# Performance work log

Hardware: AMD Instinct MI355X
Metric: run time of the kernel (lower is better)

The kernel has to match this reference:

```python
import jax, jax.numpy as jnp
import numpy as np

N, C_IN, C_OUT = 16384, 512, 1024

def setup_inputs() -> dict:
    key = jax.random.key(0)
    k1, k2 = jax.random.split(key)
    x = jax.random.normal(k1, (N, C_IN), dtype=jnp.float32)
    mean = jax.random.normal(k2, (C_OUT, C_IN), dtype=jnp.float32)
    return {"x": x, "mean": mean}

def reference(x, mean):
    # out[n, o] = 1 / sqrt(sum_c (x[n,c] - mean[o,c])^2)
    x_sq = jnp.sum(x * x, axis=-1, keepdims=True)            # [N, 1]
    m_sq = jnp.sum(mean * mean, axis=-1)                     # [O]
    cross = jnp.einsum('nc,oc->no', x, mean)                 # [N, O] GEMM
    d2 = x_sq - 2.0 * cross + m_sq[None, :]                  # [N, O]
    return jax.lax.rsqrt(d2)
```

## Files before the change

### kernel.cpp

```cpp
#include <hip/hip_runtime.h>
#include <hip/hip_bf16.h>
#include <stdint.h>

#define N_ROWS 16384
#define O_ROWS 1024
#define K_DIM  512

typedef __bf16 bf16x8 __attribute__((ext_vector_type(8)));
typedef float  f32x4  __attribute__((ext_vector_type(4)));

__device__ __forceinline__ ushort f2bfu(float f) {
    __bf16 h = (__bf16)f;
    return __builtin_bit_cast(ushort, h);
}

#define BAR_LGKM()  do {                                        \
    asm volatile("s_waitcnt lgkmcnt(0)" ::: "memory");          \
    __builtin_amdgcn_s_barrier();                               \
} while (0)

__global__ __launch_bounds__(512) void quadra_kernel(
    const float* __restrict__ x, const float* __restrict__ mean,
    float* __restrict__ out)
{
    __shared__ ushort sA[256 * 64];
    __shared__ ushort sB[128 * 64];

    const int bid  = blockIdx.x;
    const int t    = (bid & 7) * 64 + (bid >> 3);
    const int brow = (t >> 3) * 256;
    const int bcol = (t & 7) * 128;

    const int tid  = threadIdx.x;
    const int lane = tid & 63;
    const int wid  = tid >> 6;
    const int wr = wid >> 1, wc = wid & 1;

    f32x4 acc[4][4] = {};

    const int r0 = tid >> 3;
    const int q  = tid & 7;

    const float* gA = x    + (size_t)(brow + r0) * K_DIM + q * 8;
    const float* gB = mean + (size_t)(bcol + r0) * K_DIM + q * 8;

    float asq[4] = {0.f, 0.f, 0.f, 0.f};
    float bsq[2] = {0.f, 0.f};

    const int hi = lane >> 4, cl = lane & 15;

    f32x4 pa[4][2], pb[2][2];
    #pragma unroll
    for (int i = 0; i < 4; ++i) {
        const float* p = gA + (size_t)(i * 64) * K_DIM;
        pa[i][0] = *(const f32x4*)(p);
        pa[i][1] = *(const f32x4*)(p + 4);
    }
    #pragma unroll
    for (int i = 0; i < 2; ++i) {
        const float* p = gB + (size_t)(i * 64) * K_DIM;
        pb[i][0] = *(const f32x4*)(p);
        pb[i][1] = *(const f32x4*)(p + 4);
    }

    #pragma unroll 1
    for (int kt = 0; kt < 8; ++kt) {
        #pragma unroll
        for (int i = 0; i < 4; ++i) {
            f32x4 v0 = pa[i][0], v1 = pa[i][1];
            asq[i] += v0[0]*v0[0] + v0[1]*v0[1] + v0[2]*v0[2] + v0[3]*v0[3]
                    + v1[0]*v1[0] + v1[1]*v1[1] + v1[2]*v1[2] + v1[3]*v1[3];
            bf16x8 cv;
            cv[0] = (__bf16)v0[0]; cv[1] = (__bf16)v0[1];
            cv[2] = (__bf16)v0[2]; cv[3] = (__bf16)v0[3];
            cv[4] = (__bf16)v1[0]; cv[5] = (__bf16)v1[1];
            cv[6] = (__bf16)v1[2]; cv[7] = (__bf16)v1[3];
            const int row = r0 + i * 64;
            const int wb  = (q * 16) ^ ((row & 7) << 4);
            *(bf16x8*)(sA + row * 64 + (wb >> 1)) = cv;
        }
        #pragma unroll
        for (int i = 0; i < 2; ++i) {
            f32x4 v0 = pb[i][0], v1 = pb[i][1];
            bsq[i] += v0[0]*v0[0] + v0[1]*v0[1] + v0[2]*v0[2] + v0[3]*v0[3]
                    + v1[0]*v1[0] + v1[1]*v1[1] + v1[2]*v1[2] + v1[3]*v1[3];
            bf16x8 cv;
            cv[0] = (__bf16)(v0[0] * -2.0f); cv[1] = (__bf16)(v0[1] * -2.0f);
            cv[2] = (__bf16)(v0[2] * -2.0f); cv[3] = (__bf16)(v0[3] * -2.0f);
            cv[4] = (__bf16)(v1[0] * -2.0f); cv[5] = (__bf16)(v1[1] * -2.0f);
            cv[6] = (__bf16)(v1[2] * -2.0f); cv[7] = (__bf16)(v1[3] * -2.0f);
            const int row = r0 + i * 64;
            const int wb  = (q * 16) ^ ((row & 7) << 4);
            *(bf16x8*)(sB + row * 64 + (wb >> 1)) = cv;
        }

        if (kt < 7) {
            #pragma unroll
            for (int i = 0; i < 4; ++i) {
                const float* p = gA + (size_t)(i * 64) * K_DIM + (kt + 1) * 64;
                pa[i][0] = *(const f32x4*)(p);
                pa[i][1] = *(const f32x4*)(p + 4);
            }
            #pragma unroll
            for (int i = 0; i < 2; ++i) {
                const float* p = gB + (size_t)(i * 64) * K_DIM + (kt + 1) * 64;
                pb[i][0] = *(const f32x4*)(p);
                pb[i][1] = *(const f32x4*)(p + 4);
            }
        }

        BAR_LGKM();

        #pragma unroll
        for (int ks = 0; ks < 2; ++ks) {
            bf16x8 a[4], b[4];
            #pragma unroll
            for (int m = 0; m < 4; ++m) {
                const int row = wr*64 + m*16 + cl;
                const int rb  = (ks*64 + hi*16) ^ ((row & 7) << 4);
                a[m] = *(const bf16x8*)(sA + row * 64 + (rb >> 1));
            }
            #pragma unroll
            for (int n = 0; n < 4; ++n) {
                const int row = wc*64 + n*16 + cl;
                const int rb  = (ks*64 + hi*16) ^ ((row & 7) << 4);
                b[n] = *(const bf16x8*)(sB + row * 64 + (rb >> 1));
            }
            #pragma unroll
            for (int m = 0; m < 4; ++m)
                #pragma unroll
                for (int n = 0; n < 4; ++n)
                    acc[m][n] = __builtin_amdgcn_mfma_f32_16x16x32_bf16(
                        a[m], b[n], acc[m][n], 0, 0, 0);
        }

        BAR_LGKM();
    }

    ushort* sAe = sA;
    ushort* sBe = sA + 256 * 32;
    #pragma unroll
    for (int i = 0; i < 4; ++i) {
        float sa = asq[i];
        #pragma unroll
        for (int msk = 1; msk < 8; msk <<= 1) sa += __shfl_xor(sa, msk);
        uint2 aw = {0u, 0u};
        if (q == 0) aw.x = (uint32_t)f2bfu(sa) | (0x3F80u << 16);
        *(uint2*)(sAe + (r0 + i * 64) * 32 + q * 4) = aw;
    }
    #pragma unroll
    for (int i = 0; i < 2; ++i) {
        float sb = bsq[i];
        #pragma unroll
        for (int msk = 1; msk < 8; msk <<= 1) sb += __shfl_xor(sb, msk);
        uint2 bw = {0u, 0u};
        if (q == 0) bw.x = 0x3F80u | ((uint32_t)f2bfu(sb) << 16);
        *(uint2*)(sBe + (r0 + i * 64) * 32 + q * 4) = bw;
    }
    BAR_LGKM();

    {
        bf16x8 a[4], b[4];
        #pragma unroll
        for (int m = 0; m < 4; ++m)
            a[m] = *(const bf16x8*)(sAe + (wr*64 + m*16 + cl) * 32 + hi * 8);
        #pragma unroll
        for (int n = 0; n < 4; ++n)
            b[n] = *(const bf16x8*)(sBe + (wc*64 + n*16 + cl) * 32 + hi * 8);
        #pragma unroll
        for (int m = 0; m < 4; ++m)
            #pragma unroll
            for (int n = 0; n < 4; ++n)
                acc[m][n] = __builtin_amdgcn_mfma_f32_16x16x32_bf16(
                    a[m], b[n], acc[m][n], 0, 0, 0);
    }

    const int rg = lane >> 4;
    #pragma unroll
    for (int m = 0; m < 4; ++m) {
        #pragma unroll
        for (int j = 0; j < 4; ++j) {
            const int grow = brow + wr*64 + m*16 + rg*4 + j;
            float* orow = out + (size_t)grow * O_ROWS + bcol + wc*64 + cl;
            #pragma unroll
            for (int n = 0; n < 4; ++n)
                orow[n * 16] = rsqrtf(acc[m][n][j]);
        }
    }
}

extern "C" void kernel_launch(void* const* d_in, const int* in_sizes, int n_in,
                              void* d_out, int out_size, void* d_ws, size_t ws_size,
                              hipStream_t stream) {
    const float* x    = (const float*)d_in[0];
    const float* mean = (const float*)d_in[1];
    float* out = (float*)d_out;

    quadra_kernel<<<dim3((N_ROWS / 256) * (O_ROWS / 128)), 512, 0, stream>>>(
        x, mean, out);
}
```

Baseline: 49.94 us.

## Double-buffer LDS tiles and overlap next-tile conversion with MFMA

Shared-memory tiles for A and B become double-buffered. The bf16 conversion and LDS store of the next K-tile now sit between the two MFMA k-substeps of the current tile, so each iteration needs one barrier instead of two. The aim is to hide conversion and store latency behind matrix math. In exchange, LDS use per block doubles to about 96KB, which likely allows only one 512-thread block per CU instead of two and may reduce latency hiding across blocks.

```diff
diff --git a/kernel.cpp b/kernel.cpp
--- a/kernel.cpp
+++ b/kernel.cpp
@@ -23,8 +23,8 @@
     const float* __restrict__ x, const float* __restrict__ mean,
     float* __restrict__ out)
 {
-    __shared__ ushort sA[256 * 64];
-    __shared__ ushort sB[128 * 64];
+    __shared__ ushort sA[2][256 * 64];
+    __shared__ ushort sB[2][128 * 64];
 
     const int bid  = blockIdx.x;
     const int t    = (bid & 7) * 64 + (bid >> 3);
@@ -35,6 +35,7 @@
     const int lane = tid & 63;
     const int wid  = tid >> 6;
     const int wr = wid >> 1, wc = wid & 1;
+    const int cl = lane & 15, hi = lane >> 4;
 
     f32x4 acc[4][4] = {};
 
@@ -47,9 +48,8 @@
     float asq[4] = {0.f, 0.f, 0.f, 0.f};
     float bsq[2] = {0.f, 0.f};
 
-    const int hi = lane >> 4, cl = lane & 15;
-
     f32x4 pa[4][2], pb[2][2];
+
     #pragma unroll
     for (int i = 0; i < 4; ++i) {
         const float* p = gA + (size_t)(i * 64) * K_DIM;
@@ -62,37 +62,43 @@
         pb[i][0] = *(const f32x4*)(p);
         pb[i][1] = *(const f32x4*)(p + 4);
     }
+    #pragma unroll
+    for (int i = 0; i < 4; ++i) {
+        f32x4 v0 = pa[i][0], v1 = pa[i][1];
+        asq[i] += v0[0]*v0[0] + v0[1]*v0[1] + v0[2]*v0[2] + v0[3]*v0[3]
+                + v1[0]*v1[0] + v1[1]*v1[1] + v1[2]*v1[2] + v1[3]*v1[3];
+        bf16x8 cv;
+        cv[0] = (__bf16)v0[0]; cv[1] = (__bf16)v0[1];
+        cv[2] = (__bf16)v0[2]; cv[3] = (__bf16)v0[3];
+        cv[4] = (__bf16)v1[0]; cv[5] = (__bf16)v1[1];
+        cv[6] = (__bf16)v1[2]; cv[7] = (__bf16)v1[3];
+        const int row = r0 + i * 64;
+        const int wb  = (q * 16) ^ ((row & 7) << 4);
+        *(bf16x8*)(&sA[0][0] + row * 64 + (wb >> 1)) = cv;
+    }
+    #pragma unroll
+    for (int i = 0; i < 2; ++i) {
+        f32x4 v0 = pb[i][0], v1 = pb[i][1];
+        bsq[i] += v0[0]*v0[0] + v0[1]*v0[1] + v0[2]*v0[2] + v0[3]*v0[3]
+                + v1[0]*v1[0] + v1[1]*v1[1] + v1[2]*v1[2] + v1[3]*v1[3];
+        bf16x8 cv;
+        cv[0] = (__bf16)(v0[0] * -2.0f); cv[1] = (__bf16)(v0[1] * -2.0f);
+        cv[2] = (__bf16)(v0[2] * -2.0f); cv[3] = (__bf16)(v0[3] * -2.0f);
+        cv[4] = (__bf16)(v1[0] * -2.0f); cv[5] = (__bf16)(v1[1] * -2.0f);
+        cv[6] = (__bf16)(v1[2] * -2.0f); cv[7] = (__bf16)(v1[3] * -2.0f);
+        const int row = r0 + i * 64;
+        const int wb  = (q * 16) ^ ((row & 7) << 4);
+        *(bf16x8*)(&sB[0][0] + row * 64 + (wb >> 1)) = cv;
+    }
+    BAR_LGKM();
 
     #pragma unroll 1
     for (int kt = 0; kt < 8; ++kt) {
-        #pragma unroll
-        for (int i = 0; i < 4; ++i) {
-            f32x4 v0 = pa[i][0], v1 = pa[i][1];
-            asq[i] += v0[0]*v0[0] + v0[1]*v0[1] + v0[2]*v0[2] + v0[3]*v0[3]
-                    + v1[0]*v1[0] + v1[1]*v1[1] + v1[2]*v1[2] + v1[3]*v1[3];
-            bf16x8 cv;
-            cv[0] = (__bf16)v0[0]; cv[1] = (__bf16)v0[1];
-            cv[2] = (__bf16)v0[2]; cv[3] = (__bf16)v0[3];
-            cv[4] = (__bf16)v1[0]; cv[5] = (__bf16)v1[1];
-            cv[6] = (__bf16)v1[2]; cv[7] = (__bf16)v1[3];
-            const int row = r0 + i * 64;
-            const int wb  = (q * 16) ^ ((row & 7) << 4);
-            *(bf16x8*)(sA + row * 64 + (wb >> 1)) = cv;
-        }
-        #pragma unroll
-        for (int i = 0; i < 2; ++i) {
-            f32x4 v0 = pb[i][0], v1 = pb[i][1];
-            bsq[i] += v0[0]*v0[0] + v0[1]*v0[1] + v0[2]*v0[2] + v0[3]*v0[3]
-                    + v1[0]*v1[0] + v1[1]*v1[1] + v1[2]*v1[2] + v1[3]*v1[3];
-            bf16x8 cv;
-            cv[0] = (__bf16)(v0[0] * -2.0f); cv[1] = (__bf16)(v0[1] * -2.0f);
-            cv[2] = (__bf16)(v0[2] * -2.0f); cv[3] = (__bf16)(v0[3] * -2.0f);
-            cv[4] = (__bf16)(v1[0] * -2.0f); cv[5] = (__bf16)(v1[1] * -2.0f);
-            cv[6] = (__bf16)(v1[2] * -2.0f); cv[7] = (__bf16)(v1[3] * -2.0f);
-            const int row = r0 + i * 64;
-            const int wb  = (q * 16) ^ ((row & 7) << 4);
-            *(bf16x8*)(sB + row * 64 + (wb >> 1)) = cv;
-        }
+        const int cur = kt & 1;
+        ushort* bufA = &sA[cur][0];
+        ushort* bufB = &sB[cur][0];
+        ushort* nxtA = &sA[cur ^ 1][0];
+        ushort* nxtB = &sB[cur ^ 1][0];
 
         if (kt < 7) {
             #pragma unroll
@@ -109,22 +115,19 @@
             }
         }
 
-        BAR_LGKM();
-
-        #pragma unroll
-        for (int ks = 0; ks < 2; ++ks) {
+        {
             bf16x8 a[4], b[4];
             #pragma unroll
             for (int m = 0; m < 4; ++m) {
                 const int row = wr*64 + m*16 + cl;
-                const int rb  = (ks*64 + hi*16) ^ ((row & 7) << 4);
-                a[m] = *(const bf16x8*)(sA + row * 64 + (rb >> 1));
+                const int rb  = (hi*16) ^ ((row & 7) << 4);
+                a[m] = *(const bf16x8*)(bufA + row * 64 + (rb >> 1));
             }
             #pragma unroll
             for (int n = 0; n < 4; ++n) {
                 const int row = wc*64 + n*16 + cl;
-                const int rb  = (ks*64 + hi*16) ^ ((row & 7) << 4);
-                b[n] = *(const bf16x8*)(sB + row * 64 + (rb >> 1));
+                const int rb  = (hi*16) ^ ((row & 7) << 4);
+                b[n] = *(const bf16x8*)(bufB + row * 64 + (rb >> 1));
             }
             #pragma unroll
             for (int m = 0; m < 4; ++m)
@@ -134,11 +137,64 @@
                         a[m], b[n], acc[m][n], 0, 0, 0);
         }
 
+        if (kt < 7) {
+            #pragma unroll
+            for (int i = 0; i < 4; ++i) {
+                f32x4 v0 = pa[i][0], v1 = pa[i][1];
+                asq[i] += v0[0]*v0[0] + v0[1]*v0[1] + v0[2]*v0[2] + v0[3]*v0[3]
+                        + v1[0]*v1[0] + v1[1]*v1[1] + v1[2]*v1[2] + v1[3]*v1[3];
+                bf16x8 cv;
+                cv[0] = (__bf16)v0[0]; cv[1] = (__bf16)v0[1];
+                cv[2] = (__bf16)v0[2]; cv[3] = (__bf16)v0[3];
+                cv[4] = (__bf16)v1[0]; cv[5] = (__bf16)v1[1];
+                cv[6] = (__bf16)v1[2]; cv[7] = (__bf16)v1[3];
+                const int row = r0 + i * 64;
+                const int wb  = (q * 16) ^ ((row & 7) << 4);
+                *(bf16x8*)(nxtA + row * 64 + (wb >> 1)) = cv;
+            }
+            #pragma unroll
+            for (int i = 0; i < 2; ++i) {
+                f32x4 v0 = pb[i][0], v1 = pb[i][1];
+                bsq[i] += v0[0]*v0[0] + v0[1]*v0[1] + v0[2]*v0[2] + v0[3]*v0[3]
+                        + v1[0]*v1[0] + v1[1]*v1[1] + v1[2]*v1[2] + v1[3]*v1[3];
+                bf16x8 cv;
+                cv[0] = (__bf16)(v0[0] * -2.0f); cv[1] = (__bf16)(v0[1] * -2.0f);
+                cv[2] = (__bf16)(v0[2] * -2.0f); cv[3] = (__bf16)(v0[3] * -2.0f);
+                cv[4] = (__bf16)(v1[0] * -2.0f); cv[5] = (__bf16)(v1[1] * -2.0f);
+                cv[6] = (__bf16)(v1[2] * -2.0f); cv[7] = (__bf16)(v1[3] * -2.0f);
+                const int row = r0 + i * 64;
+                const int wb  = (q * 16) ^ ((row & 7) << 4);
+                *(bf16x8*)(nxtB + row * 64 + (wb >> 1)) = cv;
+            }
+        }
+
+        {
+            bf16x8 a[4], b[4];
+            #pragma unroll
+            for (int m = 0; m < 4; ++m) {
+                const int row = wr*64 + m*16 + cl;
+                const int rb  = (64 + hi*16) ^ ((row & 7) << 4);
+                a[m] = *(const bf16x8*)(bufA + row * 64 + (rb >> 1));
+            }
+            #pragma unroll
+            for (int n = 0; n < 4; ++n) {
+                const int row = wc*64 + n*16 + cl;
+                const int rb  = (64 + hi*16) ^ ((row & 7) << 4);
+                b[n] = *(const bf16x8*)(bufB + row * 64 + (rb >> 1));
+            }
+            #pragma unroll
+            for (int m = 0; m < 4; ++m)
+                #pragma unroll
+                for (int n = 0; n < 4; ++n)
+                    acc[m][n] = __builtin_amdgcn_mfma_f32_16x16x32_bf16(
+                        a[m], b[n], acc[m][n], 0, 0, 0);
+        }
+
         BAR_LGKM();
     }
 
-    ushort* sAe = sA;
-    ushort* sBe = sA + 256 * 32;
+    ushort* sAe = &sA[0][0];
+    ushort* sBe = &sA[0][0] + 256 * 32;
     #pragma unroll
     for (int i = 0; i < 4; ++i) {
         float sa = asq[i];
@@ -175,12 +231,11 @@
                     a[m], b[n], acc[m][n], 0, 0, 0);
     }
 
-    const int rg = lane >> 4;
     #pragma unroll
     for (int m = 0; m < 4; ++m) {
         #pragma unroll
         for (int j = 0; j < 4; ++j) {
-            const int grow = brow + wr*64 + m*16 + rg*4 + j;
+            const int grow = brow + wr*64 + m*16 + hi*4 + j;
             float* orow = out + (size_t)grow * O_ROWS + bcol + wc*64 + cl;
             #pragma unroll
             for (int n = 0; n < 4; ++n)
```

Measured after the change: 44.16 us. 1.13x faster.
